# Kernel optimization log

Hardware: AMD Instinct MI355X
Metric: run time of the kernel (lower is better)

The kernel has to match this reference:

```python
import jax, jax.numpy as jnp
import numpy as np

LAMBDA = 0.95   # cfg.lambda_decay
ETA = 0.5       # cfg.eta
EPS_REL = 1e-6  # cfg.epsilon (relative-error denom)
S_INNER = 3     # cfg.inner_steps
LN_EPS = 1e-5   # torch LayerNorm default eps

T, B, D_G, D_H = 48, 48, 256, 512


def setup_inputs() -> dict:
    key = jax.random.key(0)
    ks = jax.random.split(key, 5)
    # scale weights ~ kaiming/xavier so the recurrence is well-behaved
    return {
        "z_seq": jax.random.normal(ks[0], (T, B, D_G), jnp.float32),
        "clean_vec": jax.random.normal(ks[1], (B, D_G), jnp.float32),
        "W_h": jax.random.normal(ks[2], (D_H, D_H), jnp.float32) * (2.0 / D_H) ** 0.5,
        "W_g": jax.random.normal(ks[3], (D_H, D_G), jnp.float32) * (1.0 / D_G) ** 0.5,
        "b_h": jnp.zeros((D_H,), jnp.float32),
        "gamma": jnp.ones((D_H,), jnp.float32),
        "beta": jnp.zeros((D_H,), jnp.float32),
        "W_head": jax.random.normal(ks[4], (D_G, D_H), jnp.float32) * (1.0 / D_H) ** 0.5,
        "b_head": jnp.zeros((D_G,), jnp.float32),
    }


def _layernorm(x, gamma, beta):
    mu = jnp.mean(x, axis=-1, keepdims=True)
    var = jnp.mean(jnp.square(x - mu), axis=-1, keepdims=True)
    return (x - mu) * jax.lax.rsqrt(var + LN_EPS) * gamma + beta


def reference(z_seq, clean_vec, W_h, W_g, b_h, gamma, beta, W_head, b_head):
    Bsz = clean_vec.shape[0]
    d_h = W_h.shape[0]
    h0 = jnp.zeros((Bsz, d_h), z_seq.dtype)
    A0 = jnp.zeros((Bsz, d_h, d_h), z_seq.dtype)

    def step(carry, z_t):
        h_prev, A = carry
        base = h_prev @ W_h.T + z_t @ W_g.T + b_h          # (B, d_h)
        h = jax.nn.relu(_layernorm(base, gamma, beta))
        for _ in range(S_INNER):                            # inner fast-weight settling
            add_Ah = jnp.einsum('bij,bj->bi', A, h)         # bmm(A, h)
            h = jax.nn.relu(_layernorm(base + add_Ah, gamma, beta))
        A = LAMBDA * A + ETA * jnp.einsum('bi,bj->bij', h, h)  # Hebbian outer-product update
        return (h, A), None

    (h, A), _ = jax.lax.scan(step, (h0, A0), z_seq)

    pred_vec = h @ W_head.T + b_head                        # (B, d_g)
    pred_norm = pred_vec / (jnp.linalg.norm(pred_vec, axis=1, keepdims=True) + 1e-6)
    clean_norm = clean_vec / (jnp.linalg.norm(clean_vec, axis=1, keepdims=True) + 1e-6)
    sq_err = jnp.sum(jnp.square(pred_vec - clean_vec), axis=1)
    denom = jnp.sum(jnp.square(clean_vec), axis=1) + EPS_REL
    loss = jnp.mean(sq_err / denom)
    acc = jnp.mean(jnp.sum(pred_norm * clean_norm, axis=1))
    return loss, acc
```

## Files before the change

kernel.cpp:

```cpp
#include <hip/hip_runtime.h>

#define T_STEPS 48
#define BATCH   48
#define DG      256
#define DH      512
#define S_INNER 3
#define HDSTRIDE 260

typedef _Float16 hf2 __attribute__((ext_vector_type(2)));

__device__ __forceinline__ hf2 bch(unsigned u) { return __builtin_bit_cast(hf2, u); }
__device__ __forceinline__ unsigned pkh(_Float16 a, _Float16 b) {
  hf2 v{a, b}; return __builtin_bit_cast(unsigned, v);
}
__device__ __forceinline__ float fdot2u(unsigned a, unsigned b, float c) {
#if __has_builtin(__builtin_amdgcn_fdot2)
  return __builtin_amdgcn_fdot2(bch(a), bch(b), c, false);
#else
  hf2 x = bch(a), y = bch(b);
  return fmaf((float)x.x, (float)y.x, fmaf((float)x.y, (float)y.y, c));
#endif
}
template <int CTRL>
__device__ __forceinline__ float dpp_add(float v) {
  int t = __builtin_amdgcn_update_dpp(0, __float_as_int(v), CTRL, 0xf, 0xf, true);
  return v + __int_as_float(t);
}
template <int CTRL>
__device__ __forceinline__ float dpp_mov(float v) {
  return __int_as_float(
      __builtin_amdgcn_update_dpp(0, __float_as_int(v), CTRL, 0xf, 0xf, true));
}
__device__ __forceinline__ float wave64_sum63(float v) {
  v = dpp_add<0xB1>(v);
  v = dpp_add<0x4E>(v);
  v = dpp_add<0x141>(v);
  v = dpp_add<0x140>(v);
  v = dpp_add<0x142>(v);
  v = dpp_add<0x143>(v);
  return v;
}
__device__ __forceinline__ float row16_sum(float v) {
  v = dpp_add<0xB1>(v);
  v = dpp_add<0x4E>(v);
  v = dpp_add<0x141>(v);
  v = dpp_add<0x140>(v);
  return v;
}

__global__ __launch_bounds__(256)
void pack_whq(const float* __restrict__ W, uint2* __restrict__ Wq) {
  int idx = blockIdx.x * 256 + threadIdx.x;
  int j = idx & (DH - 1), q = idx >> 9;
  float w0 = W[(size_t)(4 * q + 0) * DH + j];
  float w1 = W[(size_t)(4 * q + 1) * DH + j];
  float w2 = W[(size_t)(4 * q + 2) * DH + j];
  float w3 = W[(size_t)(4 * q + 3) * DH + j];
  uint2 o;
  o.x = pkh((_Float16)w0, (_Float16)w1);
  o.y = pkh((_Float16)w2, (_Float16)w3);
  Wq[(size_t)j * 128 + q] = o;
}

__global__ __launch_bounds__(256)
void transpose_k(const float* __restrict__ in, float* __restrict__ out, int R, int C) {
  __shared__ float tile[32][33];
  int c0 = blockIdx.x * 32, r0 = blockIdx.y * 32;
  int tx = threadIdx.x & 31, ty = threadIdx.x >> 5;
  #pragma unroll
  for (int k = 0; k < 32; k += 8)
    tile[ty + k][tx] = in[(size_t)(r0 + ty + k) * C + (c0 + tx)];
  __syncthreads();
  #pragma unroll
  for (int k = 0; k < 32; k += 8)
    out[(size_t)(c0 + ty + k) * R + (r0 + tx)] = tile[tx][ty + k];
}

__global__ __launch_bounds__(DH, 2)
void zg_kernel(const float* __restrict__ z, const float* __restrict__ WgT,
               float* __restrict__ ZG) {
  const int row0 = blockIdx.x * 8;
  const int tid = threadIdx.x;
  __shared__ __align__(16) float zl[8][DG];
  for (int i = tid; i < 8 * (DG / 4); i += DH) {
    int r = i >> 6, c = i & 63;
    ((float4*)zl[r])[c] = ((const float4*)(z + (size_t)(row0 + r) * DG))[c];
  }
  __syncthreads();
  float acc[8] = {0.f, 0.f, 0.f, 0.f, 0.f, 0.f, 0.f, 0.f};
  for (int j = 0; j < DG; j += 4) {
    float w0 = WgT[(size_t)(j + 0) * DH + tid];
    float w1 = WgT[(size_t)(j + 1) * DH + tid];
    float w2 = WgT[(size_t)(j + 2) * DH + tid];
    float w3 = WgT[(size_t)(j + 3) * DH + tid];
    #pragma unroll
    for (int r = 0; r < 8; ++r) {
      float4 zz = ((const float4*)zl[r])[j >> 2];
      acc[r] = fmaf(w0, zz.x, acc[r]);
      acc[r] = fmaf(w1, zz.y, acc[r]);
      acc[r] = fmaf(w2, zz.z, acc[r]);
      acc[r] = fmaf(w3, zz.w, acc[r]);
    }
  }
  #pragma unroll
  for (int r = 0; r < 8; ++r)
    ZG[(size_t)(row0 + r) * DH + tid] = acc[r];
}

#define HCASE(s) case (2*(s)): hreg[(s)] = hb; break; \
                 case (2*(s)+1): hreg[(s)] |= (hb << 16); break;

#define MVACC(E, wA, wB) do {                                        \
    hf2 h0 = bch((E).y), h1 = bch((E).w);                            \
    a0 += bch((wA).x) * h0; a1 += bch((wA).y) * h0;                  \
    a2 += bch((wA).z) * h0; a3 += bch((wA).w) * h0;                  \
    b0 += bch((wB).x) * h1; b1 += bch((wB).y) * h1;                  \
    b2 += bch((wB).z) * h1; b3 += bch((wB).w) * h1;                  \
  } while (0)

#define LDW(off) (*(const uint4*)(Wb + ((off) + l16)))

__global__ __launch_bounds__(512, 2)
void rnn_main(const float* __restrict__ ZG, const uint2* __restrict__ Whq,
              const float* __restrict__ bh, const float* __restrict__ gamma,
              const float* __restrict__ beta, const float* __restrict__ W_head,
              const float* __restrict__ b_head, const float* __restrict__ clean,
              float* __restrict__ outbuf) {
  const int b = blockIdx.x;
  const int tid  = threadIdx.x;
  const int lane = tid & 63;
  const int wv   = tid >> 6;
  const int dim  = tid;
  const int g    = tid >> 4;
  const int dj   = tid & 15;
  const bool g16 = tid < 256;

  __shared__ __align__(16) unsigned histd[T_STEPS * HDSTRIDE];
  __shared__ __align__(16) float    pm[8 * DH];
  __shared__ __align__(16) uint2    APr[8 * 64];
  __shared__ __align__(16) unsigned h2cur[256];
  __shared__ __align__(16) unsigned cbufh2[24];
  __shared__ __align__(16) float    hcur[DH];
  __shared__ __align__(16) float    pred[DG];
  __shared__ __align__(16) float2   red[8];
  __shared__ float  red4[32];
  __shared__ int    wcntp[8];
  __shared__ float  lampow[T_STEPS];

  const float g_i  = gamma[dim];
  const float be_i = beta[dim];
  const float bh_i = bh[dim];
  if (tid == 0) {
    float pw = 0.5f;
    for (int k = 0; k < T_STEPS; ++k) { lampow[k] = pw; pw *= 0.95f; }
  }
  unsigned hreg[24];
  #pragma unroll
  for (int k = 0; k < 24; ++k) hreg[k] = 0u;

  const char* Wb = (const char*)Whq;
  const unsigned l16 = (unsigned)(lane << 4);
  __syncthreads();

  for (int t = 0; t < T_STEPS; ++t) {
    float zg = ZG[((size_t)t * BATCH + b) * DH + dim];

    uint4 hA0, hA1, hA2, hA3, hB0, hB1, hB2, hB3;
    hA0 = hA1 = hA2 = hA3 = make_uint4(0u, 0u, 0u, 0u);
    hB0 = hB1 = hB2 = hB3 = make_uint4(0u, 0u, 0u, 0u);
    if (g < t) {
      const unsigned* rpA = histd + g * HDSTRIDE + 4 * dj;
      hA0 = *(const uint4*)(rpA + 0);
      hA1 = *(const uint4*)(rpA + 64);
      hA2 = *(const uint4*)(rpA + 128);
      hA3 = *(const uint4*)(rpA + 192);
    }
    if (g16 && 32 + g < t) {
      const unsigned* rpB = histd + (32 + g) * HDSTRIDE + 4 * dj;
      hB0 = *(const uint4*)(rpB + 0);
      hB1 = *(const uint4*)(rpB + 64);
      hB2 = *(const uint4*)(rpB + 128);
      hB3 = *(const uint4*)(rpB + 192);
    }

    {
      hf2 a0{}, a1{}, a2{}, a3{}, b0{}, b1{}, b2{}, b3{};
      if (t > 0) {
        const int n = wcntp[wv];
        if (n > 0) {
          const uint4* ap4 = (const uint4*)(APr + wv * 64);
          const int G = n >> 1;
          uint4 E0 = ap4[0], E1 = ap4[1], E2 = ap4[2], E3 = ap4[3];
          uint4 wA0 = LDW(E0.x), wB0 = LDW(E0.z);
          uint4 wA1 = LDW(E1.x), wB1 = LDW(E1.z);
          uint4 wA2 = LDW(E2.x), wB2 = LDW(E2.z);
          uint4 wA3 = LDW(E3.x), wB3 = LDW(E3.z);
          for (int grp = 4; grp < G; grp += 4) {
            uint4 F0 = ap4[grp], F1 = ap4[grp + 1];
            uint4 F2 = ap4[grp + 2], F3 = ap4[grp + 3];
            uint4 xA0 = LDW(F0.x), xB0 = LDW(F0.z);
            uint4 xA1 = LDW(F1.x), xB1 = LDW(F1.z);
            uint4 xA2 = LDW(F2.x), xB2 = LDW(F2.z);
            uint4 xA3 = LDW(F3.x), xB3 = LDW(F3.z);
            MVACC(E0, wA0, wB0); MVACC(E1, wA1, wB1);
            MVACC(E2, wA2, wB2); MVACC(E3, wA3, wB3);
            E0 = F0; E1 = F1; E2 = F2; E3 = F3;
            wA0 = xA0; wB0 = xB0; wA1 = xA1; wB1 = xB1;
            wA2 = xA2; wB2 = xB2; wA3 = xA3; wB3 = xB3;
          }
          MVACC(E0, wA0, wB0); MVACC(E1, wA1, wB1);
          MVACC(E2, wA2, wB2); MVACC(E3, wA3, wB3);
        }
      }
      float4 s0, s1;
      s0.x = (float)a0.x + (float)b0.x; s0.y = (float)a0.y + (float)b0.y;
      s0.z = (float)a1.x + (float)b1.x; s0.w = (float)a1.y + (float)b1.y;
      s1.x = (float)a2.x + (float)b2.x; s1.y = (float)a2.y + (float)b2.y;
      s1.z = (float)a3.x + (float)b3.x; s1.w = (float)a3.y + (float)b3.y;
      float4* pmw = (float4*)(pm + wv * DH);
      pmw[2 * lane + 0] = s0;
      pmw[2 * lane + 1] = s1;
    }
    __syncthreads();

    float base_i = bh_i + zg;
    if (t > 0) {
      float ps = 0.f;
      #pragma unroll
      for (int sl = 0; sl < 8; ++sl) ps += pm[sl * DH + dim];
      base_i += ps;
    }

    for (int inr = 0; inr <= S_INNER; ++inr) {
      float x;
      {
        float Ah = 0.f;
        if (inr > 0 && t > 0) {
          const uint4* cbp = (const uint4*)cbufh2;
          float A0 = 0.f, A1 = 0.f, A2 = 0.f, A3 = 0.f;
          {
            uint4 c = cbp[0];
            A0 = fdot2u(hreg[0], c.x, A0); A1 = fdot2u(hreg[1], c.y, A1);
            A2 = fdot2u(hreg[2], c.z, A2); A3 = fdot2u(hreg[3], c.w, A3);
          }
          if (t > 8) {
            uint4 c = cbp[1];
            A0 = fdot2u(hreg[4], c.x, A0); A1 = fdot2u(hreg[5], c.y, A1);
            A2 = fdot2u(hreg[6], c.z, A2); A3 = fdot2u(hreg[7], c.w, A3);
          }
          if (t > 16) {
            uint4 c = cbp[2];
            A0 = fdot2u(hreg[8], c.x, A0);  A1 = fdot2u(hreg[9], c.y, A1);
            A2 = fdot2u(hreg[10], c.z, A2); A3 = fdot2u(hreg[11], c.w, A3);
          }
          if (t > 24) {
            uint4 c = cbp[3];
            A0 = fdot2u(hreg[12], c.x, A0); A1 = fdot2u(hreg[13], c.y, A1);
            A2 = fdot2u(hreg[14], c.z, A2); A3 = fdot2u(hreg[15], c.w, A3);
          }
          if (t > 32) {
            uint4 c = cbp[4];
            A0 = fdot2u(hreg[16], c.x, A0); A1 = fdot2u(hreg[17], c.y, A1);
            A2 = fdot2u(hreg[18], c.z, A2); A3 = fdot2u(hreg[19], c.w, A3);
          }
          if (t > 40) {
            uint4 c = cbp[5];
            A0 = fdot2u(hreg[20], c.x, A0); A1 = fdot2u(hreg[21], c.y, A1);
            A2 = fdot2u(hreg[22], c.z, A2); A3 = fdot2u(hreg[23], c.w, A3);
          }
          Ah = (A0 + A1) + (A2 + A3);
        }
        x = base_i + Ah;
        float sa = wave64_sum63(x);
        float sb = wave64_sum63(x * x);
        if (lane == 63) red[wv] = make_float2(sa, sb);
      }
      __syncthreads();
      float mu, rstd;
      {
        const float4* rr = (const float4*)red;
        float4 r0 = rr[0], r1 = rr[1], r2 = rr[2], r3 = rr[3];
        float s  = ((r0.x + r1.x) + (r2.x + r3.x)) + ((r0.z + r1.z) + (r2.z + r3.z));
        float s2 = ((r0.y + r1.y) + (r2.y + r3.y)) + ((r0.w + r1.w) + (r2.w + r3.w));
        const float inv = 1.f / (float)DH;
        mu = s * inv;
        float var = s2 * inv - mu * mu;
        rstd = rsqrtf(var + 1e-5f);
      }

      if (inr < S_INNER) {
        {
          float h = fmaxf(fmaf((x - mu) * rstd, g_i, be_i), 0.f);
          float hn = dpp_mov<0xB1>(h);
          if (!(dim & 1)) h2cur[dim >> 1] = pkh((_Float16)h, (_Float16)hn);
        }
        __syncthreads();
        {
          float pA = 0.f, pB = 0.f;
          if (g < t) {
            const unsigned* hp = h2cur + 4 * dj;
            uint4 v0 = *(const uint4*)(hp + 0);
            uint4 v1 = *(const uint4*)(hp + 64);
            uint4 v2 = *(const uint4*)(hp + 128);
            uint4 v3 = *(const uint4*)(hp + 192);
            float a0 = 0.f, a1 = 0.f, a2 = 0.f, a3 = 0.f;
            a0 = fdot2u(hA0.x, v0.x, a0); a1 = fdot2u(hA0.y, v0.y, a1);
            a2 = fdot2u(hA0.z, v0.z, a2); a3 = fdot2u(hA0.w, v0.w, a3);
            a0 = fdot2u(hA1.x, v1.x, a0); a1 = fdot2u(hA1.y, v1.y, a1);
            a2 = fdot2u(hA1.z, v1.z, a2); a3 = fdot2u(hA1.w, v1.w, a3);
            a0 = fdot2u(hA2.x, v2.x, a0); a1 = fdot2u(hA2.y, v2.y, a1);
            a2 = fdot2u(hA2.z, v2.z, a2); a3 = fdot2u(hA2.w, v2.w, a3);
            a0 = fdot2u(hA3.x, v3.x, a0); a1 = fdot2u(hA3.y, v3.y, a1);
            a2 = fdot2u(hA3.z, v3.z, a2); a3 = fdot2u(hA3.w, v3.w, a3);
            pA = row16_sum((a0 + a1) + (a2 + a3));
            if (g16 && 32 + g < t) {
              float e0 = 0.f, e1 = 0.f, e2 = 0.f, e3 = 0.f;
              e0 = fdot2u(hB0.x, v0.x, e0); e1 = fdot2u(hB0.y, v0.y, e1);
              e2 = fdot2u(hB0.z, v0.z, e2); e3 = fdot2u(hB0.w, v0.w, e3);
              e0 = fdot2u(hB1.x, v1.x, e0); e1 = fdot2u(hB1.y, v1.y, e1);
              e2 = fdot2u(hB1.z, v1.z, e2); e3 = fdot2u(hB1.w, v1.w, e3);
              e0 = fdot2u(hB2.x, v2.x, e0); e1 = fdot2u(hB2.y, v2.y, e1);
              e2 = fdot2u(hB2.z, v2.z, e2); e3 = fdot2u(hB2.w, v2.w, e3);
              e0 = fdot2u(hB3.x, v3.x, e0); e1 = fdot2u(hB3.y, v3.y, e1);
              e2 = fdot2u(hB3.z, v3.z, e2); e3 = fdot2u(hB3.w, v3.w, e3);
              pB = row16_sum((e0 + e1) + (e2 + e3));
            }
          }
          if (dj == 0) {
            float ccA = (g < t) ? pA * lampow[t - 1 - g] : 0.f;
            _Float16 chA = (_Float16)ccA;
            ((unsigned short*)cbufh2)[g] = __builtin_bit_cast(unsigned short, chA);
            if (g16) {
              int rB = 32 + g;
              float ccB = (rB < t) ? pB * lampow[t - 1 - rB] : 0.f;
              _Float16 chB = (_Float16)ccB;
              ((unsigned short*)cbufh2)[rB] = __builtin_bit_cast(unsigned short, chB);
            }
          }
        }
        __syncthreads();
      } else {
        {
          float h = fmaxf(fmaf((x - mu) * rstd, g_i, be_i), 0.f);
          unsigned hb = (unsigned)__builtin_bit_cast(unsigned short, (_Float16)h);
          float hn = dpp_mov<0xB1>(h);
          if (!(dim & 1))
            histd[t * HDSTRIDE + (dim >> 1)] = pkh((_Float16)h, (_Float16)hn);
          switch (t) {
            HCASE(0)  HCASE(1)  HCASE(2)  HCASE(3)  HCASE(4)  HCASE(5)
            HCASE(6)  HCASE(7)  HCASE(8)  HCASE(9)  HCASE(10) HCASE(11)
            HCASE(12) HCASE(13) HCASE(14) HCASE(15) HCASE(16) HCASE(17)
            HCASE(18) HCASE(19) HCASE(20) HCASE(21) HCASE(22) HCASE(23)
          }
          if (t == T_STEPS - 1) hcur[dim] = h;
          unsigned long long mb = __ballot(h != 0.f);
          int myoff = __popcll(mb & ((1ull << lane) - 1ull));
          int wc  = __popcll(mb);
          int wcp = (wc + 7) & ~7;
          if (h != 0.f) {
            _Float16 hh = (_Float16)h;
            uint2 ent; ent.x = (unsigned)(dim << 10); ent.y = pkh(hh, hh);
            APr[wv * 64 + myoff] = ent;
          } else {
            int inact = lane - myoff;
            if (inact < wcp - wc) {
              uint2 zz; zz.x = 0u; zz.y = 0u;
              APr[wv * 64 + wc + inact] = zz;
            }
          }
          if (lane == 0) wcntp[wv] = wcp;
        }
        __syncthreads();
      }
    }
  }

  for (int r = wv; r < DG; r += 8) {
    const float4* w4  = (const float4*)(W_head + (size_t)r * DH);
    const float4* hc4 = (const float4*)hcur;
    float4 a4 = w4[lane];      float4 c4 = hc4[lane];
    float4 a5 = w4[lane + 64]; float4 c5 = hc4[lane + 64];
    float pdot = a4.x * c4.x + a4.y * c4.y + a4.z * c4.z + a4.w * c4.w
               + a5.x * c5.x + a5.y * c5.y + a5.z * c5.z + a5.w * c5.w;
    pdot = wave64_sum63(pdot);
    if (lane == 63) pred[r] = pdot + b_head[r];
  }
  __syncthreads();

  float sq = 0.f, pc = 0.f, pp = 0.f, cc = 0.f;
  if (tid < DG) {
    float pv = pred[tid];
    float cv = clean[(size_t)b * DG + tid];
    float d = pv - cv;
    sq = d * d; pc = pv * cv; pp = pv * pv; cc = cv * cv;
  }
  #pragma unroll
  for (int off = 32; off > 0; off >>= 1) {
    sq += __shfl_xor(sq, off, 64);
    pc += __shfl_xor(pc, off, 64);
    pp += __shfl_xor(pp, off, 64);
    cc += __shfl_xor(cc, off, 64);
  }
  if (lane == 0) {
    red4[wv * 4 + 0] = sq; red4[wv * 4 + 1] = pc;
    red4[wv * 4 + 2] = pp; red4[wv * 4 + 3] = cc;
  }
  __syncthreads();
  if (tid == 0) {
    float Sq = 0.f, Pc = 0.f, Pp = 0.f, Cc = 0.f;
    #pragma unroll
    for (int w = 0; w < 8; ++w) {
      Sq += red4[w * 4 + 0]; Pc += red4[w * 4 + 1];
      Pp += red4[w * 4 + 2]; Cc += red4[w * 4 + 3];
    }
    outbuf[b]         = Sq / (Cc + 1e-6f);
    outbuf[BATCH + b] = Pc / ((sqrtf(Pp) + 1e-6f) * (sqrtf(Cc) + 1e-6f));
  }
}

__global__ __launch_bounds__(64)
void finalize_k(const float* __restrict__ outbuf, float* __restrict__ out) {
  int tid = threadIdx.x;
  float l = (tid < BATCH) ? outbuf[tid] : 0.f;
  float a = (tid < BATCH) ? outbuf[BATCH + tid] : 0.f;
  #pragma unroll
  for (int off = 32; off > 0; off >>= 1) {
    l += __shfl_xor(l, off, 64);
    a += __shfl_xor(a, off, 64);
  }
  if (tid == 0) {
    out[0] = l * (1.f / (float)BATCH);
    out[1] = a * (1.f / (float)BATCH);
  }
}

extern "C" void kernel_launch(void* const* d_in, const int* in_sizes, int n_in,
                              void* d_out, int out_size, void* d_ws, size_t ws_size,
                              hipStream_t stream) {
  (void)in_sizes; (void)n_in; (void)out_size; (void)ws_size;
  const float* z      = (const float*)d_in[0];
  const float* clean  = (const float*)d_in[1];
  const float* W_h    = (const float*)d_in[2];
  const float* W_g    = (const float*)d_in[3];
  const float* b_h    = (const float*)d_in[4];
  const float* gamma  = (const float*)d_in[5];
  const float* beta   = (const float*)d_in[6];
  const float* W_head = (const float*)d_in[7];
  const float* b_head = (const float*)d_in[8];

  float* wsf     = (float*)d_ws;
  uint2* Whq     = (uint2*)wsf;
  float* WgT     = wsf + 131072;
  float* ZG      = WgT + (size_t)DG * DH;
  float* outbuf  = ZG + (size_t)T_STEPS * BATCH * DH;

  hipLaunchKernelGGL(pack_whq, dim3(256), dim3(256), 0, stream, W_h, Whq);
  hipLaunchKernelGGL(transpose_k, dim3(DG / 32, DH / 32), dim3(256), 0, stream,
                     W_g, WgT, DH, DG);
  hipLaunchKernelGGL(zg_kernel, dim3((T_STEPS * BATCH) / 8), dim3(DH), 0, stream,
                     z, WgT, ZG);
  hipLaunchKernelGGL(rnn_main, dim3(BATCH), dim3(512), 0, stream,
                     ZG, Whq, b_h, gamma, beta, W_head, b_head, clean, outbuf);
  hipLaunchKernelGGL(finalize_k, dim3(1), dim3(64), 0, stream,
                     outbuf, (float*)d_out);
}
```

Before: 278.3 us.

## Process two batch elements per block to halve barriers per sample

Each workgroup now runs the recurrence for two batch rows at once, interleaving their matvec, layernorm reductions, Hebbian dot phases and sparse-list builds so that each __syncthreads serves both rows. The grid shrinks from 48 to 24 blocks. This is meant to amortise barrier and latency costs across two independent chains and give more instruction-level parallelism. In exchange it doubles LDS (the history buffers get close to the LDS limit) and register use (two 24-entry hreg arrays plus two prefetch sets), and it uses only 24 CUs, so the serial chain per block gets longer.

```diff
diff --git a/kernel.cpp b/kernel.cpp
--- a/kernel.cpp
+++ b/kernel.cpp
@@ -107,8 +107,9 @@
     ZG[(size_t)(row0 + r) * DH + tid] = acc[r];
 }
 
-#define HCASE(s) case (2*(s)): hreg[(s)] = hb; break; \
-                 case (2*(s)+1): hreg[(s)] |= (hb << 16); break;
+#define HCASE2(s) \
+  case (2*(s)):   hreg0[(s)] = hb0;          hreg1[(s)] = hb1;          break; \
+  case (2*(s)+1): hreg0[(s)] |= (hb0 << 16); hreg1[(s)] |= (hb1 << 16); break;
 
 #define MVACC(E, wA, wB) do {                                        \
     hf2 h0 = bch((E).y), h1 = bch((E).w);                            \
@@ -120,13 +121,121 @@
 
 #define LDW(off) (*(const uint4*)(Wb + ((off) + l16)))
 
+__device__ __forceinline__ float compute_ah(const unsigned (&hreg)[24],
+                                            const unsigned* cbuf, int t) {
+  const uint4* cbp = (const uint4*)cbuf;
+  float A0 = 0.f, A1 = 0.f, A2 = 0.f, A3 = 0.f;
+  {
+    uint4 c = cbp[0];
+    A0 = fdot2u(hreg[0], c.x, A0); A1 = fdot2u(hreg[1], c.y, A1);
+    A2 = fdot2u(hreg[2], c.z, A2); A3 = fdot2u(hreg[3], c.w, A3);
+  }
+  if (t > 8) {
+    uint4 c = cbp[1];
+    A0 = fdot2u(hreg[4], c.x, A0); A1 = fdot2u(hreg[5], c.y, A1);
+    A2 = fdot2u(hreg[6], c.z, A2); A3 = fdot2u(hreg[7], c.w, A3);
+  }
+  if (t > 16) {
+    uint4 c = cbp[2];
+    A0 = fdot2u(hreg[8], c.x, A0);  A1 = fdot2u(hreg[9], c.y, A1);
+    A2 = fdot2u(hreg[10], c.z, A2); A3 = fdot2u(hreg[11], c.w, A3);
+  }
+  if (t > 24) {
+    uint4 c = cbp[3];
+    A0 = fdot2u(hreg[12], c.x, A0); A1 = fdot2u(hreg[13], c.y, A1);
+    A2 = fdot2u(hreg[14], c.z, A2); A3 = fdot2u(hreg[15], c.w, A3);
+  }
+  if (t > 32) {
+    uint4 c = cbp[4];
+    A0 = fdot2u(hreg[16], c.x, A0); A1 = fdot2u(hreg[17], c.y, A1);
+    A2 = fdot2u(hreg[18], c.z, A2); A3 = fdot2u(hreg[19], c.w, A3);
+  }
+  if (t > 40) {
+    uint4 c = cbp[5];
+    A0 = fdot2u(hreg[20], c.x, A0); A1 = fdot2u(hreg[21], c.y, A1);
+    A2 = fdot2u(hreg[22], c.z, A2); A3 = fdot2u(hreg[23], c.w, A3);
+  }
+  return (A0 + A1) + (A2 + A3);
+}
+
+__device__ __forceinline__ void prefetch_rows(const unsigned* hist, int g, bool g16,
+                                              int t, int dj,
+                                              uint4 (&hA)[4], uint4 (&hB)[4]) {
+  #pragma unroll
+  for (int k = 0; k < 4; ++k) {
+    hA[k] = make_uint4(0u, 0u, 0u, 0u);
+    hB[k] = make_uint4(0u, 0u, 0u, 0u);
+  }
+  if (g < t) {
+    const unsigned* rp = hist + g * HDSTRIDE + 4 * dj;
+    hA[0] = *(const uint4*)(rp + 0);
+    hA[1] = *(const uint4*)(rp + 64);
+    hA[2] = *(const uint4*)(rp + 128);
+    hA[3] = *(const uint4*)(rp + 192);
+  }
+  if (g16 && 32 + g < t) {
+    const unsigned* rp = hist + (32 + g) * HDSTRIDE + 4 * dj;
+    hB[0] = *(const uint4*)(rp + 0);
+    hB[1] = *(const uint4*)(rp + 64);
+    hB[2] = *(const uint4*)(rp + 128);
+    hB[3] = *(const uint4*)(rp + 192);
+  }
+}
+
+__device__ __forceinline__ void dot_phase(const unsigned* h2c,
+                                          const uint4 (&hA)[4], const uint4 (&hB)[4],
+                                          bool g16, int g, int t, int dj,
+                                          const float* lampow, unsigned* cbuf) {
+  float pA = 0.f, pB = 0.f;
+  if (g < t) {
+    const unsigned* hp = h2c + 4 * dj;
+    uint4 v0 = *(const uint4*)(hp + 0);
+    uint4 v1 = *(const uint4*)(hp + 64);
+    uint4 v2 = *(const uint4*)(hp + 128);
+    uint4 v3 = *(const uint4*)(hp + 192);
+    float a0 = 0.f, a1 = 0.f, a2 = 0.f, a3 = 0.f;
+    a0 = fdot2u(hA[0].x, v0.x, a0); a1 = fdot2u(hA[0].y, v0.y, a1);
+    a2 = fdot2u(hA[0].z, v0.z, a2); a3 = fdot2u(hA[0].w, v0.w, a3);
+    a0 = fdot2u(hA[1].x, v1.x, a0); a1 = fdot2u(hA[1].y, v1.y, a1);
+    a2 = fdot2u(hA[1].z, v1.z, a2); a3 = fdot2u(hA[1].w, v1.w, a3);
+    a0 = fdot2u(hA[2].x, v2.x, a0); a1 = fdot2u(hA[2].y, v2.y, a1);
+    a2 = fdot2u(hA[2].z, v2.z, a2); a3 = fdot2u(hA[2].w, v2.w, a3);
+    a0 = fdot2u(hA[3].x, v3.x, a0); a1 = fdot2u(hA[3].y, v3.y, a1);
+    a2 = fdot2u(hA[3].z, v3.z, a2); a3 = fdot2u(hA[3].w, v3.w, a3);
+    pA = row16_sum((a0 + a1) + (a2 + a3));
+    if (g16 && 32 + g < t) {
+      float e0 = 0.f, e1 = 0.f, e2 = 0.f, e3 = 0.f;
+      e0 = fdot2u(hB[0].x, v0.x, e0); e1 = fdot2u(hB[0].y, v0.y, e1);
+      e2 = fdot2u(hB[0].z, v0.z, e2); e3 = fdot2u(hB[0].w, v0.w, e3);
+      e0 = fdot2u(hB[1].x, v1.x, e0); e1 = fdot2u(hB[1].y, v1.y, e1);
+      e2 = fdot2u(hB[1].z, v1.z, e2); e3 = fdot2u(hB[1].w, v1.w, e3);
+      e0 = fdot2u(hB[2].x, v2.x, e0); e1 = fdot2u(hB[2].y, v2.y, e1);
+      e2 = fdot2u(hB[2].z, v2.z, e2); e3 = fdot2u(hB[2].w, v2.w, e3);
+      e0 = fdot2u(hB[3].x, v3.x, e0); e1 = fdot2u(hB[3].y, v3.y, e1);
+      e2 = fdot2u(hB[3].z, v3.z, e2); e3 = fdot2u(hB[3].w, v3.w, e3);
+      pB = row16_sum((e0 + e1) + (e2 + e3));
+    }
+  }
+  if (dj == 0) {
+    float ccA = (g < t) ? pA * lampow[t - 1 - g] : 0.f;
+    _Float16 chA = (_Float16)ccA;
+    ((unsigned short*)cbuf)[g] = __builtin_bit_cast(unsigned short, chA);
+    if (g16) {
+      int rB = 32 + g;
+      float ccB = (rB < t) ? pB * lampow[t - 1 - rB] : 0.f;
+      _Float16 chB = (_Float16)ccB;
+      ((unsigned short*)cbuf)[rB] = __builtin_bit_cast(unsigned short, chB);
+    }
+  }
+}
+
 __global__ __launch_bounds__(512, 2)
 void rnn_main(const float* __restrict__ ZG, const uint2* __restrict__ Whq,
               const float* __restrict__ bh, const float* __restrict__ gamma,
               const float* __restrict__ beta, const float* __restrict__ W_head,
               const float* __restrict__ b_head, const float* __restrict__ clean,
               float* __restrict__ outbuf) {
-  const int b = blockIdx.x;
+  const int bat0 = blockIdx.x * 2, bat1 = bat0 + 1;
   const int tid  = threadIdx.x;
   const int lane = tid & 63;
   const int wv   = tid >> 6;
@@ -135,16 +244,16 @@
   const int dj   = tid & 15;
   const bool g16 = tid < 256;
 
-  __shared__ __align__(16) unsigned histd[T_STEPS * HDSTRIDE];
-  __shared__ __align__(16) float    pm[8 * DH];
-  __shared__ __align__(16) uint2    APr[8 * 64];
-  __shared__ __align__(16) unsigned h2cur[256];
-  __shared__ __align__(16) unsigned cbufh2[24];
-  __shared__ __align__(16) float    hcur[DH];
-  __shared__ __align__(16) float    pred[DG];
-  __shared__ __align__(16) float2   red[8];
-  __shared__ float  red4[32];
-  __shared__ int    wcntp[8];
+  __shared__ __align__(16) unsigned histd[2][T_STEPS * HDSTRIDE];
+  __shared__ __align__(16) float    pm[2][8 * DH];
+  __shared__ __align__(16) uint2    APr[2][8 * 64];
+  __shared__ __align__(16) unsigned h2cur[2][256];
+  __shared__ __align__(16) unsigned cbufh2[2][32];
+  __shared__ __align__(16) float    hcur[2][DH];
+  __shared__ __align__(16) float    pred[2][DG];
+  __shared__ __align__(16) float2   red[2][8];
+  __shared__ float  red4[2][32];
+  __shared__ int    wcntp[2][8];
   __shared__ float  lampow[T_STEPS];
 
   const float g_i  = gamma[dim];
@@ -154,41 +263,28 @@
     float pw = 0.5f;
     for (int k = 0; k < T_STEPS; ++k) { lampow[k] = pw; pw *= 0.95f; }
   }
-  unsigned hreg[24];
-  #pragma unroll
-  for (int k = 0; k < 24; ++k) hreg[k] = 0u;
+  unsigned hreg0[24], hreg1[24];
+  #pragma unroll
+  for (int k = 0; k < 24; ++k) { hreg0[k] = 0u; hreg1[k] = 0u; }
 
   const char* Wb = (const char*)Whq;
   const unsigned l16 = (unsigned)(lane << 4);
   __syncthreads();
 
   for (int t = 0; t < T_STEPS; ++t) {
-    float zg = ZG[((size_t)t * BATCH + b) * DH + dim];
-
-    uint4 hA0, hA1, hA2, hA3, hB0, hB1, hB2, hB3;
-    hA0 = hA1 = hA2 = hA3 = make_uint4(0u, 0u, 0u, 0u);
-    hB0 = hB1 = hB2 = hB3 = make_uint4(0u, 0u, 0u, 0u);
-    if (g < t) {
-      const unsigned* rpA = histd + g * HDSTRIDE + 4 * dj;
-      hA0 = *(const uint4*)(rpA + 0);
-      hA1 = *(const uint4*)(rpA + 64);
-      hA2 = *(const uint4*)(rpA + 128);
-      hA3 = *(const uint4*)(rpA + 192);
-    }
-    if (g16 && 32 + g < t) {
-      const unsigned* rpB = histd + (32 + g) * HDSTRIDE + 4 * dj;
-      hB0 = *(const uint4*)(rpB + 0);
-      hB1 = *(const uint4*)(rpB + 64);
-      hB2 = *(const uint4*)(rpB + 128);
-      hB3 = *(const uint4*)(rpB + 192);
-    }
-
-    {
+    float zg0 = ZG[((size_t)t * BATCH + bat0) * DH + dim];
+    float zg1 = ZG[((size_t)t * BATCH + bat1) * DH + dim];
+
+    uint4 hA0[4], hB0[4], hA1[4], hB1[4];
+    prefetch_rows(histd[0], g, g16, t, dj, hA0, hB0);
+
+    #pragma unroll
+    for (int bb = 0; bb < 2; ++bb) {
       hf2 a0{}, a1{}, a2{}, a3{}, b0{}, b1{}, b2{}, b3{};
       if (t > 0) {
-        const int n = wcntp[wv];
+        const int n = wcntp[bb][wv];
         if (n > 0) {
-          const uint4* ap4 = (const uint4*)(APr + wv * 64);
+          const uint4* ap4 = (const uint4*)(APr[bb] + wv * 64);
           const int G = n >> 1;
           uint4 E0 = ap4[0], E1 = ap4[1], E2 = ap4[2], E3 = ap4[3];
           uint4 wA0 = LDW(E0.x), wB0 = LDW(E0.z);
@@ -217,204 +313,188 @@
       s0.z = (float)a1.x + (float)b1.x; s0.w = (float)a1.y + (float)b1.y;
       s1.x = (float)a2.x + (float)b2.x; s1.y = (float)a2.y + (float)b2.y;
       s1.z = (float)a3.x + (float)b3.x; s1.w = (float)a3.y + (float)b3.y;
-      float4* pmw = (float4*)(pm + wv * DH);
+      float4* pmw = (float4*)(pm[bb] + wv * DH);
       pmw[2 * lane + 0] = s0;
       pmw[2 * lane + 1] = s1;
     }
+    prefetch_rows(histd[1], g, g16, t, dj, hA1, hB1);
     __syncthreads();
 
-    float base_i = bh_i + zg;
+    float base0 = bh_i + zg0, base1 = bh_i + zg1;
     if (t > 0) {
-      float ps = 0.f;
+      float p0 = 0.f, p1 = 0.f;
       #pragma unroll
-      for (int sl = 0; sl < 8; ++sl) ps += pm[sl * DH + dim];
-      base_i += ps;
+      for (int sl = 0; sl < 8; ++sl) {
+        p0 += pm[0][sl * DH + dim];
+        p1 += pm[1][sl * DH + dim];
+      }
+      base0 += p0; base1 += p1;
     }
 
     for (int inr = 0; inr <= S_INNER; ++inr) {
-      float x;
+      float x0, x1;
       {
-        float Ah = 0.f;
+        float Ah0 = 0.f, Ah1 = 0.f;
         if (inr > 0 && t > 0) {
-          const uint4* cbp = (const uint4*)cbufh2;
-          float A0 = 0.f, A1 = 0.f, A2 = 0.f, A3 = 0.f;
-          {
-            uint4 c = cbp[0];
-            A0 = fdot2u(hreg[0], c.x, A0); A1 = fdot2u(hreg[1], c.y, A1);
-            A2 = fdot2u(hreg[2], c.z, A2); A3 = fdot2u(hreg[3], c.w, A3);
-          }
-          if (t > 8) {
-            uint4 c = cbp[1];
-            A0 = fdot2u(hreg[4], c.x, A0); A1 = fdot2u(hreg[5], c.y, A1);
-            A2 = fdot2u(hreg[6], c.z, A2); A3 = fdot2u(hreg[7], c.w, A3);
-          }
-          if (t > 16) {
-            uint4 c = cbp[2];
-            A0 = fdot2u(hreg[8], c.x, A0);  A1 = fdot2u(hreg[9], c.y, A1);
-            A2 = fdot2u(hreg[10], c.z, A2); A3 = fdot2u(hreg[11], c.w, A3);
-          }
-          if (t > 24) {
-            uint4 c = cbp[3];
-            A0 = fdot2u(hreg[12], c.x, A0); A1 = fdot2u(hreg[13], c.y, A1);
-            A2 = fdot2u(hreg[14], c.z, A2); A3 = fdot2u(hreg[15], c.w, A3);
-          }
-          if (t > 32) {
-            uint4 c = cbp[4];
-            A0 = fdot2u(hreg[16], c.x, A0); A1 = fdot2u(hreg[17], c.y, A1);
-            A2 = fdot2u(hreg[18], c.z, A2); A3 = fdot2u(hreg[19], c.w, A3);
-          }
-          if (t > 40) {
-            uint4 c = cbp[5];
-            A0 = fdot2u(hreg[20], c.x, A0); A1 = fdot2u(hreg[21], c.y, A1);
-            A2 = fdot2u(hreg[22], c.z, A2); A3 = fdot2u(hreg[23], c.w, A3);
-          }
-          Ah = (A0 + A1) + (A2 + A3);
+          Ah0 = compute_ah(hreg0, cbufh2[0], t);
+          Ah1 = compute_ah(hreg1, cbufh2[1], t);
         }
-        x = base_i + Ah;
-        float sa = wave64_sum63(x);
-        float sb = wave64_sum63(x * x);
-        if (lane == 63) red[wv] = make_float2(sa, sb);
+        x0 = base0 + Ah0;
+        x1 = base1 + Ah1;
+        float sa0 = wave64_sum63(x0);
+        float sb0 = wave64_sum63(x0 * x0);
+        float sa1 = wave64_sum63(x1);
+        float sb1 = wave64_sum63(x1 * x1);
+        if (lane == 63) {
+          red[0][wv] = make_float2(sa0, sb0);
+          red[1][wv] = make_float2(sa1, sb1);
+        }
       }
       __syncthreads();
-      float mu, rstd;
+      float mu0, rstd0, mu1, rstd1;
       {
-        const float4* rr = (const float4*)red;
+        const float4* rr = (const float4*)red[0];
         float4 r0 = rr[0], r1 = rr[1], r2 = rr[2], r3 = rr[3];
         float s  = ((r0.x + r1.x) + (r2.x + r3.x)) + ((r0.z + r1.z) + (r2.z + r3.z));
         float s2 = ((r0.y + r1.y) + (r2.y + r3.y)) + ((r0.w + r1.w) + (r2.w + r3.w));
         const float inv = 1.f / (float)DH;
-        mu = s * inv;
-        float var = s2 * inv - mu * mu;
-        rstd = rsqrtf(var + 1e-5f);
+        mu0 = s * inv;
+        rstd0 = rsqrtf(s2 * inv - mu0 * mu0 + 1e-5f);
+      }
+      {
+        const float4* rr = (const float4*)red[1];
+        float4 r0 = rr[0], r1 = rr[1], r2 = rr[2], r3 = rr[3];
+        float s  = ((r0.x + r1.x) + (r2.x + r3.x)) + ((r0.z + r1.z) + (r2.z + r3.z));
+        float s2 = ((r0.y + r1.y) + (r2.y + r3.y)) + ((r0.w + r1.w) + (r2.w + r3.w));
+        const float inv = 1.f / (float)DH;
+        mu1 = s * inv;
+        rstd1 = rsqrtf(s2 * inv - mu1 * mu1 + 1e-5f);
       }
 
       if (inr < S_INNER) {
         {
-          float h = fmaxf(fmaf((x - mu) * rstd, g_i, be_i), 0.f);
-          float hn = dpp_mov<0xB1>(h);
-          if (!(dim & 1)) h2cur[dim >> 1] = pkh((_Float16)h, (_Float16)hn);
-        }
-        __syncthreads();
-        {
-          float pA = 0.f, pB = 0.f;
-          if (g < t) {
-            const unsigned* hp = h2cur + 4 * dj;
-            uint4 v0 = *(const uint4*)(hp + 0);
-            uint4 v1 = *(const uint4*)(hp + 64);
-            uint4 v2 = *(const uint4*)(hp + 128);
-            uint4 v3 = *(const uint4*)(hp + 192);
-            float a0 = 0.f, a1 = 0.f, a2 = 0.f, a3 = 0.f;
-            a0 = fdot2u(hA0.x, v0.x, a0); a1 = fdot2u(hA0.y, v0.y, a1);
-            a2 = fdot2u(hA0.z, v0.z, a2); a3 = fdot2u(hA0.w, v0.w, a3);
-            a0 = fdot2u(hA1.x, v1.x, a0); a1 = fdot2u(hA1.y, v1.y, a1);
-            a2 = fdot2u(hA1.z, v1.z, a2); a3 = fdot2u(hA1.w, v1.w, a3);
-            a0 = fdot2u(hA2.x, v2.x, a0); a1 = fdot2u(hA2.y, v2.y, a1);
-            a2 = fdot2u(hA2.z, v2.z, a2); a3 = fdot2u(hA2.w, v2.w, a3);
-            a0 = fdot2u(hA3.x, v3.x, a0); a1 = fdot2u(hA3.y, v3.y, a1);
-            a2 = fdot2u(hA3.z, v3.z, a2); a3 = fdot2u(hA3.w, v3.w, a3);
-            pA = row16_sum((a0 + a1) + (a2 + a3));
-            if (g16 && 32 + g < t) {
-              float e0 = 0.f, e1 = 0.f, e2 = 0.f, e3 = 0.f;
-              e0 = fdot2u(hB0.x, v0.x, e0); e1 = fdot2u(hB0.y, v0.y, e1);
-              e2 = fdot2u(hB0.z, v0.z, e2); e3 = fdot2u(hB0.w, v0.w, e3);
-              e0 = fdot2u(hB1.x, v1.x, e0); e1 = fdot2u(hB1.y, v1.y, e1);
-              e2 = fdot2u(hB1.z, v1.z, e2); e3 = fdot2u(hB1.w, v1.w, e3);
-              e0 = fdot2u(hB2.x, v2.x, e0); e1 = fdot2u(hB2.y, v2.y, e1);
-              e2 = fdot2u(hB2.z, v2.z, e2); e3 = fdot2u(hB2.w, v2.w, e3);
-              e0 = fdot2u(hB3.x, v3.x, e0); e1 = fdot2u(hB3.y, v3.y, e1);
-              e2 = fdot2u(hB3.z, v3.z, e2); e3 = fdot2u(hB3.w, v3.w, e3);
-              pB = row16_sum((e0 + e1) + (e2 + e3));
-            }
-          }
-          if (dj == 0) {
-            float ccA = (g < t) ? pA * lampow[t - 1 - g] : 0.f;
-            _Float16 chA = (_Float16)ccA;
-            ((unsigned short*)cbufh2)[g] = __builtin_bit_cast(unsigned short, chA);
-            if (g16) {
-              int rB = 32 + g;
-              float ccB = (rB < t) ? pB * lampow[t - 1 - rB] : 0.f;
-              _Float16 chB = (_Float16)ccB;
-              ((unsigned short*)cbufh2)[rB] = __builtin_bit_cast(unsigned short, chB);
-            }
+          float h0 = fmaxf(fmaf((x0 - mu0) * rstd0, g_i, be_i), 0.f);
+          float h1 = fmaxf(fmaf((x1 - mu1) * rstd1, g_i, be_i), 0.f);
+          float hn0 = dpp_mov<0xB1>(h0);
+          float hn1 = dpp_mov<0xB1>(h1);
+          if (!(dim & 1)) {
+            h2cur[0][dim >> 1] = pkh((_Float16)h0, (_Float16)hn0);
+            h2cur[1][dim >> 1] = pkh((_Float16)h1, (_Float16)hn1);
           }
         }
         __syncthreads();
+        dot_phase(h2cur[0], hA0, hB0, g16, g, t, dj, lampow, cbufh2[0]);
+        dot_phase(h2cur[1], hA1, hB1, g16, g, t, dj, lampow, cbufh2[1]);
+        __syncthreads();
       } else {
         {
-          float h = fmaxf(fmaf((x - mu) * rstd, g_i, be_i), 0.f);
-          unsigned hb = (unsigned)__builtin_bit_cast(unsigned short, (_Float16)h);
-          float hn = dpp_mov<0xB1>(h);
-          if (!(dim & 1))
-            histd[t * HDSTRIDE + (dim >> 1)] = pkh((_Float16)h, (_Float16)hn);
+          float h0 = fmaxf(fmaf((x0 - mu0) * rstd0, g_i, be_i), 0.f);
+          float h1 = fmaxf(fmaf((x1 - mu1) * rstd1, g_i, be_i), 0.f);
+          unsigned hb0 = (unsigned)__builtin_bit_cast(unsigned short, (_Float16)h0);
+          unsigned hb1 = (unsigned)__builtin_bit_cast(unsigned short, (_Float16)h1);
+          float hn0 = dpp_mov<0xB1>(h0);
+          float hn1 = dpp_mov<0xB1>(h1);
+          if (!(dim & 1)) {
+            histd[0][t * HDSTRIDE + (dim >> 1)] = pkh((_Float16)h0, (_Float16)hn0);
+            histd[1][t * HDSTRIDE + (dim >> 1)] = pkh((_Float16)h1, (_Float16)hn1);
+          }
           switch (t) {
-            HCASE(0)  HCASE(1)  HCASE(2)  HCASE(3)  HCASE(4)  HCASE(5)
-            HCASE(6)  HCASE(7)  HCASE(8)  HCASE(9)  HCASE(10) HCASE(11)
-            HCASE(12) HCASE(13) HCASE(14) HCASE(15) HCASE(16) HCASE(17)
-            HCASE(18) HCASE(19) HCASE(20) HCASE(21) HCASE(22) HCASE(23)
+            HCASE2(0)  HCASE2(1)  HCASE2(2)  HCASE2(3)  HCASE2(4)  HCASE2(5)
+            HCASE2(6)  HCASE2(7)  HCASE2(8)  HCASE2(9)  HCASE2(10) HCASE2(11)
+            HCASE2(12) HCASE2(13) HCASE2(14) HCASE2(15) HCASE2(16) HCASE2(17)
+            HCASE2(18) HCASE2(19) HCASE2(20) HCASE2(21) HCASE2(22) HCASE2(23)
           }
-          if (t == T_STEPS - 1) hcur[dim] = h;
-          unsigned long long mb = __ballot(h != 0.f);
-          int myoff = __popcll(mb & ((1ull << lane) - 1ull));
-          int wc  = __popcll(mb);
-          int wcp = (wc + 7) & ~7;
-          if (h != 0.f) {
-            _Float16 hh = (_Float16)h;
-            uint2 ent; ent.x = (unsigned)(dim << 10); ent.y = pkh(hh, hh);
-            APr[wv * 64 + myoff] = ent;
-          } else {
-            int inact = lane - myoff;
-            if (inact < wcp - wc) {
-              uint2 zz; zz.x = 0u; zz.y = 0u;
-              APr[wv * 64 + wc + inact] = zz;
+          if (t == T_STEPS - 1) { hcur[0][dim] = h0; hcur[1][dim] = h1; }
+          {
+            unsigned long long mb = __ballot(h0 != 0.f);
+            int myoff = __popcll(mb & ((1ull << lane) - 1ull));
+            int wc  = __popcll(mb);
+            int wcp = (wc + 7) & ~7;
+            if (h0 != 0.f) {
+              _Float16 hh = (_Float16)h0;
+              uint2 ent; ent.x = (unsigned)(dim << 10); ent.y = pkh(hh, hh);
+              APr[0][wv * 64 + myoff] = ent;
+            } else {
+              int inact = lane - myoff;
+              if (inact < wcp - wc) {
+                uint2 zz; zz.x = 0u; zz.y = 0u;
+                APr[0][wv * 64 + wc + inact] = zz;
+              }
             }
+            if (lane == 0) wcntp[0][wv] = wcp;
           }
-          if (lane == 0) wcntp[wv] = wcp;
+          {
+            unsigned long long mb = __ballot(h1 != 0.f);
+            int myoff = __popcll(mb & ((1ull << lane) - 1ull));
+            int wc  = __popcll(mb);
+            int wcp = (wc + 7) & ~7;
+            if (h1 != 0.f) {
+              _Float16 hh = (_Float16)h1;
+              uint2 ent; ent.x = (unsigned)(dim << 10); ent.y = pkh(hh, hh);
+              APr[1][wv * 64 + myoff] = ent;
+            } else {
+              int inact = lane - myoff;
+              if (inact < wcp - wc) {
+                uint2 zz; zz.x = 0u; zz.y = 0u;
+                APr[1][wv * 64 + wc + inact] = zz;
+              }
+            }
+            if (lane == 0) wcntp[1][wv] = wcp;
+          }
         }
         __syncthreads();
       }
     }
   }
 
-  for (int r = wv; r < DG; r += 8) {
-    const float4* w4  = (const float4*)(W_head + (size_t)r * DH);
-    const float4* hc4 = (const float4*)hcur;
-    float4 a4 = w4[lane];      float4 c4 = hc4[lane];
-    float4 a5 = w4[lane + 64]; float4 c5 = hc4[lane + 64];
-    float pdot = a4.x * c4.x + a4.y * c4.y + a4.z * c4.z + a4.w * c4.w
-               + a5.x * c5.x + a5.y * c5.y + a5.z * c5.z + a5.w * c5.w;
-    pdot = wave64_sum63(pdot);
-    if (lane == 63) pred[r] = pdot + b_head[r];
+  #pragma unroll
+  for (int bb = 0; bb < 2; ++bb) {
+    for (int r = wv; r < DG; r += 8) {
+      const float4* w4  = (const float4*)(W_head + (size_t)r * DH);
+      const float4* hc4 = (const float4*)hcur[bb];
+      float4 a4 = w4[lane];      float4 c4 = hc4[lane];
+      float4 a5 = w4[lane + 64]; float4 c5 = hc4[lane + 64];
+      float pdot = a4.x * c4.x + a4.y * c4.y + a4.z * c4.z + a4.w * c4.w
+                 + a5.x * c5.x + a5.y * c5.y + a5.z * c5.z + a5.w * c5.w;
+      pdot = wave64_sum63(pdot);
+      if (lane == 63) pred[bb][r] = pdot + b_head[r];
+    }
   }
   __syncthreads();
 
-  float sq = 0.f, pc = 0.f, pp = 0.f, cc = 0.f;
-  if (tid < DG) {
-    float pv = pred[tid];
-    float cv = clean[(size_t)b * DG + tid];
-    float d = pv - cv;
-    sq = d * d; pc = pv * cv; pp = pv * pv; cc = cv * cv;
-  }
-  #pragma unroll
-  for (int off = 32; off > 0; off >>= 1) {
-    sq += __shfl_xor(sq, off, 64);
-    pc += __shfl_xor(pc, off, 64);
-    pp += __shfl_xor(pp, off, 64);
-    cc += __shfl_xor(cc, off, 64);
-  }
-  if (lane == 0) {
-    red4[wv * 4 + 0] = sq; red4[wv * 4 + 1] = pc;
-    red4[wv * 4 + 2] = pp; red4[wv * 4 + 3] = cc;
+  #pragma unroll
+  for (int bb = 0; bb < 2; ++bb) {
+    const int bat = (bb == 0) ? bat0 : bat1;
+    float sq = 0.f, pc = 0.f, pp = 0.f, cc = 0.f;
+    if (tid < DG) {
+      float pv = pred[bb][tid];
+      float cv = clean[(size_t)bat * DG + tid];
+      float d = pv - cv;
+      sq = d * d; pc = pv * cv; pp = pv * pv; cc = cv * cv;
+    }
+    #pragma unroll
+    for (int off = 32; off > 0; off >>= 1) {
+      sq += __shfl_xor(sq, off, 64);
+      pc += __shfl_xor(pc, off, 64);
+      pp += __shfl_xor(pp, off, 64);
+      cc += __shfl_xor(cc, off, 64);
+    }
+    if (lane == 0) {
+      red4[bb][wv * 4 + 0] = sq; red4[bb][wv * 4 + 1] = pc;
+      red4[bb][wv * 4 + 2] = pp; red4[bb][wv * 4 + 3] = cc;
+    }
   }
   __syncthreads();
-  if (tid == 0) {
+  if (tid < 2) {
+    const int bat = (tid == 0) ? bat0 : bat1;
     float Sq = 0.f, Pc = 0.f, Pp = 0.f, Cc = 0.f;
     #pragma unroll
     for (int w = 0; w < 8; ++w) {
-      Sq += red4[w * 4 + 0]; Pc += red4[w * 4 + 1];
-      Pp += red4[w * 4 + 2]; Cc += red4[w * 4 + 3];
-    }
-    outbuf[b]         = Sq / (Cc + 1e-6f);
-    outbuf[BATCH + b] = Pc / ((sqrtf(Pp) + 1e-6f) * (sqrtf(Cc) + 1e-6f));
+      Sq += red4[tid][w * 4 + 0]; Pc += red4[tid][w * 4 + 1];
+      Pp += red4[tid][w * 4 + 2]; Cc += red4[tid][w * 4 + 3];
+    }
+    outbuf[bat]         = Sq / (Cc + 1e-6f);
+    outbuf[BATCH + bat] = Pc / ((sqrtf(Pp) + 1e-6f) * (sqrtf(Cc) + 1e-6f));
   }
 }
 
@@ -459,7 +539,7 @@
                      W_g, WgT, DH, DG);
   hipLaunchKernelGGL(zg_kernel, dim3((T_STEPS * BATCH) / 8), dim3(DH), 0, stream,
                      z, WgT, ZG);
-  hipLaunchKernelGGL(rnn_main, dim3(BATCH), dim3(512), 0, stream,
+  hipLaunchKernelGGL(rnn_main, dim3(BATCH / 2), dim3(512), 0, stream,
                      ZG, Whq, b_h, gamma, beta, W_head, b_head, clean, outbuf);
   hipLaunchKernelGGL(finalize_k, dim3(1), dim3(64), 0, stream,
                      outbuf, (float*)d_out);
```

Result: slower. 594.4 us (+113.6%).
